# Kernel optimization log

Hardware: AMD Instinct MI355X
Metric: run time of the kernel (lower is better)

The kernel has to match this reference:

```python
import jax, jax.numpy as jnp
import numpy as np

B, C, H, W0, W1 = 2, 96, 64, 128, 128
NL, K, R = 2, 4, 6  # num_layers, cross-scan directions, dt_rank = ceil(C/16)
PNAMES = ['norm_w','norm_b','in_proj_w','conv_w','x_proj_w','dt_w','dt_b','A_logs','Ds',
          'out_norm_w','out_norm_b','out_proj_w','norm2_w','norm2_b','fc1_w','fc1_b','fc2_w','fc2_b']


def setup_inputs() -> dict:
    key = jax.random.key(0)
    ks = iter(jax.random.split(key, 40))
    def rn(shape, s=0.02):
        return jax.random.normal(next(ks), shape, jnp.float32) * s
    return dict(
        x0=jax.random.normal(next(ks), (B, C, H, W0), jnp.float32),
        x1=jax.random.normal(next(ks), (B, C, H, W1), jnp.float32),
        norm_w=jnp.ones((NL, C)), norm_b=jnp.zeros((NL, C)),
        in_proj_w=rn((NL, C, C)),                 # SS2D in_proj (Linear2d, bias=False)
        conv_w=rn((NL, C, 1, 3, 3), 0.1),         # depthwise 3x3, bias=False
        x_proj_w=rn((NL, K, R + 2, C)),           # dt_rank + 2*d_state rows (d_state=1)
        dt_w=rn((NL, K, C, R), 0.1),
        dt_b=rn((NL, K, C), 0.1),
        A_logs=jnp.zeros((NL, K, C)),             # v0 init with d_state=1 -> log(1)=0
        Ds=jnp.ones((NL, K, C)),
        out_norm_w=jnp.ones((NL, C)), out_norm_b=jnp.zeros((NL, C)),
        out_proj_w=rn((NL, C, C)),                # bias=False
        norm2_w=jnp.ones((NL, C)), norm2_b=jnp.zeros((NL, C)),
        fc1_w=rn((NL, 4 * C, C)), fc1_b=jnp.zeros((NL, 4 * C)),
        fc2_w=rn((NL, C, 4 * C)), fc2_b=jnp.zeros((NL, C)),
    )


def ln2d(x, w, b, eps=1e-5):
    # LayerNorm2d: normalize over channel dim of NCHW
    mu = x.mean(1, keepdims=True)
    var = ((x - mu) ** 2).mean(1, keepdims=True)
    return (x - mu) * jax.lax.rsqrt(var + eps) * w[None, :, None, None] + b[None, :, None, None]


def conv1x1(x, w):  # Linear2d: w (out,in)
    return jnp.einsum('bchw,dc->bdhw', x, w)


def dwconv3(x, w):  # depthwise 3x3, SAME padding
    return jax.lax.conv_general_dilated(x, w, (1, 1), 'SAME',
        dimension_numbers=('NCHW', 'OIHW', 'NCHW'), feature_group_count=x.shape[1])


def linear_scan(a, b):
    # h_t = a_t * h_{t-1} + b_t along last axis, via associative scan
    def comb(l, r):
        al, bl = l
        ar, br = r
        return (ar * al, ar * bl + br)
    return jax.lax.associative_scan(comb, (a, b), axis=-1)[1]


def ss2d(x, p):
    # SS2Dv2 forward_type='v05_noz', channel_first, d_state=1
    Bs_, Cd, Hh, Ww = x.shape
    Ll = Hh * Ww
    x = conv1x1(x, p['in_proj_w'])
    x = jax.nn.silu(dwconv3(x, p['conv_w']))
    # CrossScan: row-major, col-major, and their flips -> (B,K,C,L)
    xs0 = x.reshape(Bs_, Cd, Ll)
    xs1 = x.transpose(0, 1, 3, 2).reshape(Bs_, Cd, Ll)
    xs = jnp.stack([xs0, xs1, xs0[..., ::-1], xs1[..., ::-1]], 1)
    xdbl = jnp.einsum('bkcl,kdc->bkdl', xs, p['x_proj_w'])
    dts, Bmat, Cmat = xdbl[:, :, :R], xdbl[:, :, R:R + 1], xdbl[:, :, R + 1:R + 2]
    delta = jax.nn.softplus(jnp.einsum('bkrl,kcr->bkcl', dts, p['dt_w']) + p['dt_b'][None, :, :, None])
    A = -jnp.exp(p['A_logs'])                       # (K,C), scalar state
    a = jnp.exp(delta * A[None, :, :, None])        # (B,K,C,L)
    bterm = delta * Bmat * xs                       # Bmat broadcasts over C (d_state=1)
    h = linear_scan(a, bterm)
    ys = Cmat * h + p['Ds'][None, :, :, None] * xs  # (B,K,C,L)
    # CrossMerge: un-flip dirs 2,3; map col-major back to row-major; sum
    y_row = ys[:, 0] + ys[:, 2, :, ::-1]
    y_col = ys[:, 1] + ys[:, 3, :, ::-1]
    y_col = y_col.reshape(Bs_, Cd, Ww, Hh).transpose(0, 1, 3, 2).reshape(Bs_, Cd, Ll)
    y = (y_row + y_col).reshape(Bs_, Cd, Hh, Ww)
    y = ln2d(y, p['out_norm_w'], p['out_norm_b'])
    return conv1x1(y, p['out_proj_w'])


def block(x, p):
    # drop_path is identity in eval mode; all dropout rates are 0
    x = x + ss2d(ln2d(x, p['norm_w'], p['norm_b']), p)
    h = conv1x1(ln2d(x, p['norm2_w'], p['norm2_b']), p['fc1_w']) + p['fc1_b'][None, :, None, None]
    h = jax.nn.gelu(h, approximate=False)
    return x + conv1x1(h, p['fc2_w']) + p['fc2_b'][None, :, None, None]


def run_stack(x, params):
    for i in range(NL):
        p = {k: v[i] for k, v in params.items()}
        x = block(x, p)
    return x


def _forward(x0, x1, params):
    x = jnp.concatenate([x0, x1], -1)
    xb = x[..., ::-1]
    x = run_stack(x, params)
    xb = run_stack(xb, params)
    xbf = xb[..., ::-1]
    w0 = x0.shape[-1]
    y0 = 0.5 * (x[..., :w0] + xbf[..., :w0])
    y1 = 0.5 * (x[..., w0:] + xbf[..., w0:])
    return (y0, y1)


def reference(x0, x1, norm_w, norm_b, in_proj_w, conv_w, x_proj_w, dt_w, dt_b, A_logs, Ds,
              out_norm_w, out_norm_b, out_proj_w, norm2_w, norm2_b, fc1_w, fc1_b, fc2_w, fc2_b):
    params = dict(zip(PNAMES, [norm_w, norm_b, in_proj_w, conv_w, x_proj_w, dt_w, dt_b, A_logs, Ds,
                               out_norm_w, out_norm_b, out_proj_w, norm2_w, norm2_b, fc1_w, fc1_b, fc2_w, fc2_b]))
    return _forward(x0, x1, params)
```

## Files before the change

kernel.cpp:

```cpp
#include <hip/hip_runtime.h>
#include <cstdint>
#include <cstddef>

#define BT 4
#define CC 96
#define HH 64
#define WW 256
#define LL (HH*WW)
#define KD 4
#define RR 6
#define NLAY 2
#define C4 (4*CC)
#define SLOTF 47424
#define STPW 2048

typedef unsigned short u16;
typedef __attribute__((ext_vector_type(8))) short bf16x8;
typedef __attribute__((ext_vector_type(4))) float f32x4;

__device__ __forceinline__ u16 f2bf(float f){
  unsigned u = __float_as_uint(f);
  unsigned r = (u + 0x7FFFu + ((u >> 16) & 1u)) >> 16;
  return (u16)r;
}
__device__ __forceinline__ float bf2f(u16 h){
  return __uint_as_float(((unsigned)h) << 16);
}
__device__ __forceinline__ unsigned pk_bf16(float lo, float hi){
  unsigned r;
  asm volatile("v_cvt_pk_bf16_f32 %0, %1, %2" : "=v"(r) : "v"(lo), "v"(hi));
  return r;
}
__device__ __forceinline__ float fexp2(float x){
  float r; asm("v_exp_f32 %0, %1" : "=v"(r) : "v"(x)); return r;
}
__device__ __forceinline__ float flog2(float x){
  float r; asm("v_log_f32 %0, %1" : "=v"(r) : "v"(x)); return r;
}
__device__ __forceinline__ float gelu_f(float v){
  float t = v*v;
  float u = v*fmaf(0.0356774081f, t, 0.7978845608f);
  float e2 = __expf(2.f*u);
  float r = __builtin_amdgcn_rcpf(e2 + 1.f);
  return fmaf(-v, r, v);
}

__global__ void k_build(const float* __restrict__ x0, const float* __restrict__ x1,
                        float* __restrict__ X){
  size_t i = (size_t)blockIdx.x*256 + threadIdx.x;
  size_t tot = (size_t)2*CC*HH*WW;
  if (i >= tot) return;
  int w = i % WW; size_t r = i / WW;
  int h = r % HH; size_t bc = r / HH;
  float val;
  if (w < 128) val = x0[(bc*HH + h)*128 + w];
  else         val = x1[(bc*HH + h)*128 + (w-128)];
  X[i] = val;
  size_t ib = ((bc + (size_t)2*CC)*HH + h)*WW + (WW-1-w);
  X[ib] = val;
}

template<bool ST, typename T>
__global__ __launch_bounds__(256) void k_pack(const T* __restrict__ src,
      u16* __restrict__ dst, float* __restrict__ st){
  __shared__ float tl[CC][33];
  int tid = threadIdx.x;
  int l0 = blockIdx.x*32, b = blockIdx.y;
  for (int e = tid; e < CC*32; e += 256){
    int c = e >> 5, dl = e & 31;
    T raw = src[((size_t)b*CC + c)*LL + l0 + dl];
    float vv;
    if constexpr (sizeof(T) == 2) vv = bf2f((u16)raw); else vv = (float)raw;
    tl[c][dl] = vv;
  }
  __syncthreads();
  if (ST && tid < 32){
    float s = 0.f, ss = 0.f;
    for (int c = 0; c < CC; ++c){ float vv = tl[c][tid]; s += vv; ss += vv*vv; }
    float mu = s*(1.f/CC);
    float var = ss*(1.f/CC) - mu*mu;
    st[(size_t)b*LL + l0 + tid] = mu;
    st[(size_t)BT*LL + (size_t)b*LL + l0 + tid] = rsqrtf(var + 1e-5f);
  }
  int dl = tid >> 3, cg = tid & 7;
  u16* dp = dst + ((size_t)b*LL + l0 + dl)*104 + cg*12;
  #pragma unroll
  for (int q = 0; q < 3; ++q){
    ushort4 pk;
    pk.x = f2bf(tl[cg*12 + q*4 + 0][dl]);
    pk.y = f2bf(tl[cg*12 + q*4 + 1][dl]);
    pk.z = f2bf(tl[cg*12 + q*4 + 2][dl]);
    pk.w = f2bf(tl[cg*12 + q*4 + 3][dl]);
    *(ushort4*)(dp + q*4) = pk;
  }
}

template<int M, int K, bool FC1ORD, bool LNF, bool BIAS>
__global__ void k_prepw(const float* __restrict__ W, const float* __restrict__ lnw,
      const float* __restrict__ lnb, const float* __restrict__ bias,
      u16* __restrict__ Wb, float* __restrict__ s1, float* __restrict__ cadd){
  int lay = blockIdx.y;
  W += (size_t)lay*M*K;
  Wb += (size_t)lay*SLOTF*2;
  s1 += (size_t)lay*SLOTF;
  cadd += (size_t)lay*SLOTF;
  int m = blockIdx.x*64 + threadIdx.x;
  if (m >= M) return;
  int rowfrag = m >> 4, lr = m & 15;
  float s1v = 0.f, sbv = 0.f;
  for (int c = 0; c < K; ++c){
    float wv = W[(size_t)m*K + c];
    float wf = LNF ? wv*lnw[lay*K + c] : wv;
    u16 h = f2bf(wf);
    int colfrag = c >> 5, lg = (c >> 3) & 3, j = c & 7;
    int f;
    if (FC1ORD) f = (rowfrag/6)*18 + colfrag*6 + (rowfrag % 6);
    else        f = colfrag*(M/16) + rowfrag;
    Wb[(size_t)(f*64 + lg*16 + lr)*8 + j] = h;
    s1v += bf2f(h);
    if (LNF) sbv = fmaf(wv, lnb[lay*K + c], sbv);
  }
  if (BIAS) sbv += bias[lay*M + m];
  s1[m] = s1v;
  cadd[m] = sbv;
}

template<bool LNF, bool RES, bool WF32, bool WBF, bool STATS>
__global__ __launch_bounds__(256) void k_gmm2(
    const u16* __restrict__ Wb, const u16* __restrict__ inT,
    float* __restrict__ outF, u16* __restrict__ outT,
    const float* __restrict__ s1v, const float* __restrict__ cadd,
    const float* __restrict__ res,
    const float* __restrict__ stI, float* __restrict__ stO){
  __shared__ u16 bt[128*104];
  int tid = threadIdx.x, lane = tid & 63, wid = tid >> 6;
  int l0 = blockIdx.x*128;
  int lr = lane & 15, lg = lane >> 4;
  const int4* bsrc = (const int4*)(inT + (size_t)l0*104);
  for (int i = tid; i < 1664; i += 256) ((int4*)bt)[i] = bsrc[i];
  __syncthreads();
  f32x4 acc[6][2];
  #pragma unroll
  for (int mf = 0; mf < 6; ++mf){ acc[mf][0] = (f32x4){0,0,0,0}; acc[mf][1] = (f32x4){0,0,0,0}; }
  #pragma unroll
  for (int ks = 0; ks < 3; ++ks){
    bf16x8 af[6];
    #pragma unroll
    for (int mf = 0; mf < 6; ++mf)
      af[mf] = *(const bf16x8*)(Wb + (size_t)((ks*6 + mf)*64 + lane)*8);
    bf16x8 bfr[2];
    #pragma unroll
    for (int ls = 0; ls < 2; ++ls)
      bfr[ls] = *(const bf16x8*)&bt[(wid*32 + ls*16 + lr)*104 + ks*32 + lg*8];
    #pragma unroll
    for (int mf = 0; mf < 6; ++mf)
      #pragma unroll
      for (int ls = 0; ls < 2; ++ls)
        acc[mf][ls] = __builtin_amdgcn_mfma_f32_16x16x32_bf16(af[mf], bfr[ls], acc[mf][ls], 0, 0, 0);
  }
  #pragma unroll
  for (int ls = 0; ls < 2; ++ls){
    int l = l0 + wid*32 + ls*16 + lr;
    int b = l >> 14, lb = l & (LL-1);
    float mu = 0.f, rs = 0.f;
    if (LNF){ mu = stI[l]; rs = stI[(size_t)BT*LL + l]; }
    float ssum = 0.f, ssq = 0.f;
    #pragma unroll
    for (int mf = 0; mf < 6; ++mf){
      float o[4];
      #pragma unroll
      for (int r = 0; r < 4; ++r){
        int mm = mf*16 + lg*4 + r;
        float vv = acc[mf][ls][r];
        if (LNF) vv = fmaf(rs, vv, fmaf(-mu*rs, s1v[mm], cadd[mm]));
        else     vv += cadd[mm];
        if (RES) vv += res[((size_t)b*96 + mm)*LL + lb];
        if (WF32) outF[((size_t)b*96 + mm)*LL + lb] = vv;
        if (STATS){ ssum += vv; ssq += vv*vv; }
        o[r] = vv;
      }
      if (WBF){
        ushort4 pk;
        pk.x = f2bf(o[0]); pk.y = f2bf(o[1]); pk.z = f2bf(o[2]); pk.w = f2bf(o[3]);
        *(ushort4*)(outT + (size_t)l*104 + mf*16 + lg*4) = pk;
      }
    }
    if (STATS){
      ssum += __shfl_xor(ssum, 16); ssq += __shfl_xor(ssq, 16);
      ssum += __shfl_xor(ssum, 32); ssq += __shfl_xor(ssq, 32);
      if (lane < 16){
        float mu2 = ssum*(1.f/CC);
        float var = ssq*(1.f/CC) - mu2*mu2;
        stO[l] = mu2;
        stO[(size_t)BT*LL + l] = rsqrtf(var + 1e-5f);
      }
    }
  }
}

__global__ __launch_bounds__(512, 4) void k_mlp(
    const u16* __restrict__ Wb1, const u16* __restrict__ Wb2,
    const u16* __restrict__ XT, float* __restrict__ X, u16* __restrict__ XTout,
    const float* __restrict__ s11, const float* __restrict__ c1,
    const float* __restrict__ c2,
    const float* __restrict__ stI, float* __restrict__ stO){
  __shared__ u16 bt[128*104];
  __shared__ u16 hs[128*104];
  int tid = threadIdx.x, lane = tid & 63, wid = tid >> 6;
  int l0 = blockIdx.x*128;
  int lr = lane & 15, lg = lane >> 4;
  const int4* bsrc = (const int4*)(XT + (size_t)l0*104);
  for (int i = tid; i < 1664; i += 512) ((int4*)bt)[i] = bsrc[i];

  int l = l0 + wid*16 + lr;
  float mu = stI[l];
  float rs = stI[(size_t)BT*LL + l];
  float nmr = -mu*rs;
  __syncthreads();

  int hrow = (wid*16 + lr)*104;
  f32x4 acc2[6];
  #pragma unroll
  for (int mf = 0; mf < 6; ++mf) acc2[mf] = (f32x4){0,0,0,0};

  for (int cc = 0; cc < 4; ++cc){
    f32x4 acc1[6];
    #pragma unroll
    for (int mf = 0; mf < 6; ++mf) acc1[mf] = (f32x4){0,0,0,0};
    #pragma unroll
    for (int ks = 0; ks < 3; ++ks){
      bf16x8 af[6];
      #pragma unroll
      for (int mf = 0; mf < 6; ++mf)
        af[mf] = *(const bf16x8*)(Wb1 + (size_t)((cc*18 + ks*6 + mf)*64 + lane)*8);
      bf16x8 bfr = *(const bf16x8*)&bt[hrow + ks*32 + lg*8];
      #pragma unroll
      for (int mf = 0; mf < 6; ++mf)
        acc1[mf] = __builtin_amdgcn_mfma_f32_16x16x32_bf16(af[mf], bfr, acc1[mf], 0, 0, 0);
    }
    #pragma unroll
    for (int mf = 0; mf < 6; ++mf){
      float4 sv = *(const float4*)&s11[cc*96 + mf*16 + lg*4];
      float4 cv = *(const float4*)&c1 [cc*96 + mf*16 + lg*4];
      float g0 = gelu_f(fmaf(rs, acc1[mf][0], fmaf(nmr, sv.x, cv.x)));
      float g1 = gelu_f(fmaf(rs, acc1[mf][1], fmaf(nmr, sv.y, cv.y)));
      float g2 = gelu_f(fmaf(rs, acc1[mf][2], fmaf(nmr, sv.z, cv.z)));
      float g3 = gelu_f(fmaf(rs, acc1[mf][3], fmaf(nmr, sv.w, cv.w)));
      uint2 pw;
      pw.x = pk_bf16(g0, g1);
      pw.y = pk_bf16(g2, g3);
      *(uint2*)&hs[hrow + mf*16 + lg*4] = pw;
    }
    #pragma unroll
    for (int ks = 0; ks < 3; ++ks){
      bf16x8 a2[6];
      #pragma unroll
      for (int mf2 = 0; mf2 < 6; ++mf2)
        a2[mf2] = *(const bf16x8*)(Wb2 + (size_t)(((cc*3 + ks)*6 + mf2)*64 + lane)*8);
      bf16x8 bfr2 = *(const bf16x8*)&hs[hrow + ks*32 + lg*8];
      #pragma unroll
      for (int mf2 = 0; mf2 < 6; ++mf2)
        acc2[mf2] = __builtin_amdgcn_mfma_f32_16x16x32_bf16(a2[mf2], bfr2, acc2[mf2], 0, 0, 0);
    }
  }
  {
    int b = l >> 14, lb = l & (LL-1);
    float ssum = 0.f, ssq = 0.f;
    #pragma unroll
    for (int mf = 0; mf < 6; ++mf){
      float o[4];
      #pragma unroll
      for (int r = 0; r < 4; ++r){
        int mm = mf*16 + lg*4 + r;
        float vv = acc2[mf][r] + c2[mm];
        vv += X[((size_t)b*96 + mm)*LL + lb];
        X[((size_t)b*96 + mm)*LL + lb] = vv;
        ssum += vv; ssq += vv*vv;
        o[r] = vv;
      }
      ushort4 pk;
      pk.x = f2bf(o[0]); pk.y = f2bf(o[1]); pk.z = f2bf(o[2]); pk.w = f2bf(o[3]);
      *(ushort4*)(XTout + (size_t)l*104 + mf*16 + lg*4) = pk;
    }
    ssum += __shfl_xor(ssum, 16); ssq += __shfl_xor(ssq, 16);
    ssum += __shfl_xor(ssum, 32); ssq += __shfl_xor(ssq, 32);
    if (lane < 16){
      float mu2 = ssum*(1.f/CC);
      float var = ssq*(1.f/CC) - mu2*mu2;
      stO[l] = mu2;
      stO[(size_t)BT*LL + l] = rsqrtf(var + 1e-5f);
    }
  }
}

__global__ __launch_bounds__(256) void k_dwconv_silu_t(const float* __restrict__ u,
      float* __restrict__ v, float* __restrict__ vT, const float* __restrict__ cw){
  __shared__ float tl[32][33];
  int bc = blockIdx.z;
  int c = bc % CC;
  int w0 = blockIdx.x*32, h0 = blockIdx.y*32;
  const float* up = u + (size_t)bc*LL;
  const float* k9 = cw + c*9;
  int t = threadIdx.x;
  int wl = (t & 7)*4, hl = t >> 3;
  int h = h0 + hl, w = w0 + wl;
  float acc[4] = {0.f,0.f,0.f,0.f};
  #pragma unroll
  for (int dh = -1; dh <= 1; ++dh){
    int h2 = h + dh;
    if (h2 < 0 || h2 >= HH) continue;
    const float* row = up + (size_t)h2*WW + w;
    float4 m = *(const float4*)row;
    float lft = (w > 0) ? row[-1] : 0.f;
    float rgt = (w + 4 < WW) ? row[4] : 0.f;
    float k0 = k9[(dh+1)*3], k1 = k9[(dh+1)*3+1], k2 = k9[(dh+1)*3+2];
    acc[0] += lft*k0 + m.x*k1 + m.y*k2;
    acc[1] += m.x*k0 + m.y*k1 + m.z*k2;
    acc[2] += m.y*k0 + m.z*k1 + m.w*k2;
    acc[3] += m.z*k0 + m.w*k1 + rgt*k2;
  }
  float4 ov;
  float* po = (float*)&ov;
  #pragma unroll
  for (int j = 0; j < 4; ++j){
    float a = acc[j];
    float e = __expf(-a);
    float s = a * __builtin_amdgcn_rcpf(1.f + e);
    po[j] = s;
    tl[wl + j][hl] = s;
  }
  *(float4*)&v[(size_t)bc*LL + (size_t)h*WW + w] = ov;
  __syncthreads();
  int ww = t >> 3, hh4 = (t & 7)*4;
  float4 o2 = make_float4(tl[ww][hh4], tl[ww][hh4+1], tl[ww][hh4+2], tl[ww][hh4+3]);
  *(float4*)&vT[(size_t)bc*LL + (size_t)(w0 + ww)*HH + h0 + hh4] = o2;
}

__global__ void k_xproj(const float* __restrict__ v, const float* __restrict__ vT,
                        float* __restrict__ G, const float* __restrict__ xpw){
  int which = blockIdx.y;
  const float* src = which ? vT : v;
  int kA = which ? 1 : 0, kB = which ? 3 : 2;
  size_t i = (size_t)blockIdx.x*256 + threadIdx.x;
  if (i >= (size_t)BT*LL) return;
  int b = (int)(i / LL), l = (int)(i % LL);
  const float* sp = src + (size_t)b*CC*LL + l;
  const float* wA = xpw + (size_t)kA*8*CC;
  const float* wB = xpw + (size_t)kB*8*CC;
  float aA[8], aB[8];
  #pragma unroll
  for (int d = 0; d < 8; ++d){ aA[d] = 0.f; aB[d] = 0.f; }
  for (int c = 0; c < CC; ++c){
    float xv = sp[(size_t)c*LL];
    #pragma unroll
    for (int d = 0; d < 8; ++d){
      aA[d] = fmaf(wA[d*CC + c], xv, aA[d]);
      aB[d] = fmaf(wB[d*CC + c], xv, aB[d]);
    }
  }
  float* gA = G + (((size_t)b*KD + kA)*8)*LL + l;
  float* gB = G + (((size_t)b*KD + kB)*8)*LL + l;
  #pragma unroll
  for (int d = 0; d < 8; ++d){ gA[(size_t)d*LL] = aA[d]; gB[(size_t)d*LL] = aB[d]; }
}

__device__ __forceinline__ void ld4(const float* p, float* o){
  float4 t = *(const float4*)p; o[0]=t.x; o[1]=t.y; o[2]=t.z; o[3]=t.w;
}
__device__ __forceinline__ void rev4(float* a){
  float t0 = a[0]; a[0] = a[3]; a[3] = t0;
  float t1 = a[1]; a[1] = a[2]; a[2] = t1;
}

__global__ __launch_bounds__(256) void k_scan3(const float* __restrict__ G,
                       const float* __restrict__ v, const float* __restrict__ vT,
                       u16* __restrict__ Y,
                       const float* __restrict__ dtw_, const float* __restrict__ dtb_,
                       const float* __restrict__ Alog_, const float* __restrict__ Ds_){
  const size_t SZ = (size_t)BT*CC*LL;
  const float LOG2E = 1.4426950408889634f, LN2 = 0.6931471805599453f;
  int wid = threadIdx.x >> 6, lane = threadIdx.x & 63;
  int tile = blockIdx.x*4 + wid;
  int sy = blockIdx.y;
  bool rev = (blockIdx.z != 0);
  int c = sy % CC; int t2 = sy / CC; int kk = t2 & 1; int b = t2 >> 1;
  int k = (rev ? 2 : 0) + kk;
  const float* src = (kk ? vT : v) + ((size_t)b*CC + c)*LL;
  const float* g = G + (((size_t)b*KD + k)*8)*LL;
  float dtw[RR];
  #pragma unroll
  for (int r = 0; r < RR; ++r) dtw[r] = dtw_[((size_t)k*CC + c)*RR + r];
  float dtb = dtb_[k*CC + c];
  float A  = -__expf(Alog_[k*CC + c]);
  float Dv = Ds_[k*CC + c];
  u16* yout = Y + (size_t)k*SZ + ((size_t)b*CC + c)*LL;

  int lstore0 = tile*STPW;
  float carry = 0.f;
  for (int p = 0; p < 1 + STPW/256; ++p){
    int base = lstore0 - 256 + p*256;
    if (base < 0) continue;
    bool st = (base >= lstore0);
    int l = base + (lane<<2);
    int ga = rev ? (LL-4-l) : l;
    float r0[4], r1[4], r2[4], r3[4], r4[4], r5[4], g6b[4], g7b[4], xb[4];
    ld4(g + 0*(size_t)LL + ga, r0);
    ld4(g + 1*(size_t)LL + ga, r1);
    ld4(g + 2*(size_t)LL + ga, r2);
    ld4(g + 3*(size_t)LL + ga, r3);
    ld4(g + 4*(size_t)LL + ga, r4);
    ld4(g + 5*(size_t)LL + ga, r5);
    ld4(g + 6*(size_t)LL + ga, g6b);
    if (st) ld4(g + 7*(size_t)LL + ga, g7b);
    else { g7b[0]=0.f; g7b[1]=0.f; g7b[2]=0.f; g7b[3]=0.f; }
    ld4(src + ga, xb);
    if (rev){
      rev4(r0); rev4(r1); rev4(r2); rev4(r3); rev4(r4); rev4(r5);
      rev4(g6b); rev4(g7b); rev4(xb);
    }
    float av[4], bt[4];
    #pragma unroll
    for (int i = 0; i < 4; ++i){
      float dsum = dtb;
      dsum = fmaf(r0[i], dtw[0], dsum);
      dsum = fmaf(r1[i], dtw[1], dsum);
      dsum = fmaf(r2[i], dtw[2], dsum);
      dsum = fmaf(r3[i], dtw[3], dsum);
      dsum = fmaf(r4[i], dtw[4], dsum);
      dsum = fmaf(r5[i], dtw[5], dsum);
      float dl2 = dsum*LOG2E;
      float y = flog2(1.f + fexp2(dl2));
      y = (dsum > 20.f) ? dl2 : y;
      float delta = y*LN2;
      av[i] = fexp2(A*y);
      bt[i] = delta * g6b[i] * xb[i];
    }
    float P = av[0], Q = bt[0];
    #pragma unroll
    for (int i = 1; i < 4; ++i){ Q = fmaf(av[i], Q, bt[i]); P *= av[i]; }
    #pragma unroll
    for (int off = 1; off < 64; off <<= 1){
      float Pp = __shfl_up(P, (unsigned)off);
      float Qp = __shfl_up(Q, (unsigned)off);
      if (lane >= off){ Q = fmaf(P, Qp, Q); P *= Pp; }
    }
    float Pe = __shfl_up(P, 1u), Qe = __shfl_up(Q, 1u);
    if (lane == 0){ Pe = 1.f; Qe = 0.f; }
    float h = fmaf(Pe, carry, Qe);
    if (st){
      float ys[4];
      #pragma unroll
      for (int i = 0; i < 4; ++i){
        h = fmaf(av[i], h, bt[i]);
        ys[i] = fmaf(g7b[i], h, Dv*xb[i]);
      }
      carry = __shfl(h, 63);
      if (rev) rev4(ys);
      uint2 pw;
      pw.x = pk_bf16(ys[0], ys[1]);
      pw.y = pk_bf16(ys[2], ys[3]);
      *(uint2*)&yout[ga] = pw;
    } else {
      #pragma unroll
      for (int i = 0; i < 4; ++i) h = fmaf(av[i], h, bt[i]);
      carry = __shfl(h, 63);
    }
  }
}

__global__ __launch_bounds__(256) void k_combine4(const u16* __restrict__ Y, u16* __restrict__ z){
  const size_t SZ = (size_t)BT*CC*LL;
  __shared__ float tl[64][65];
  int bc = blockIdx.z;
  int w0 = blockIdx.x*64;
  int t = threadIdx.x;
  const u16* y1p = Y + SZ   + (size_t)bc*LL;
  const u16* y3p = Y + 3*SZ + (size_t)bc*LL;
  {
    int wl = t >> 2;
    int h0 = (t & 3)*16;
    size_t base = (size_t)(w0 + wl)*HH + h0;
    #pragma unroll
    for (int j = 0; j < 4; ++j){
      ushort4 a = *(const ushort4*)&y1p[base + j*4];
      ushort4 bq = *(const ushort4*)&y3p[base + j*4];
      tl[wl][h0 + j*4 + 0] = bf2f(a.x) + bf2f(bq.x);
      tl[wl][h0 + j*4 + 1] = bf2f(a.y) + bf2f(bq.y);
      tl[wl][h0 + j*4 + 2] = bf2f(a.z) + bf2f(bq.z);
      tl[wl][h0 + j*4 + 3] = bf2f(a.w) + bf2f(bq.w);
    }
  }
  __syncthreads();
  const u16* y0p = Y +        (size_t)bc*LL;
  const u16* y2p = Y + 2*SZ + (size_t)bc*LL;
  u16* zp = z + (size_t)bc*LL;
  {
    int h = t >> 2;
    int wq = (t & 3)*16;
    #pragma unroll
    for (int j = 0; j < 4; ++j){
      int wl = wq + j*4;
      size_t idx = (size_t)h*WW + w0 + wl;
      ushort4 a = *(const ushort4*)&y0p[idx];
      ushort4 bq = *(const ushort4*)&y2p[idx];
      ushort4 o;
      o.x = f2bf(bf2f(a.x) + bf2f(bq.x) + tl[wl+0][h]);
      o.y = f2bf(bf2f(a.y) + bf2f(bq.y) + tl[wl+1][h]);
      o.z = f2bf(bf2f(a.z) + bf2f(bq.z) + tl[wl+2][h]);
      o.w = f2bf(bf2f(a.w) + bf2f(bq.w) + tl[wl+3][h]);
      *(ushort4*)&zp[idx] = o;
    }
  }
}

__global__ void k_output(const float* __restrict__ X, float* __restrict__ out){
  size_t i = (size_t)blockIdx.x*256 + threadIdx.x;
  size_t half = (size_t)2*CC*HH*128;
  if (i >= half) return;
  int w = i % 128; size_t r = i / 128;
  int h = r % HH; size_t bc = r / HH;
  size_t fwd = (bc*HH + h)*WW;
  size_t bwd = ((bc + (size_t)2*CC)*HH + h)*WW;
  out[i]        = 0.5f*(X[fwd + w]       + X[bwd + (WW-1-w)]);
  out[half + i] = 0.5f*(X[fwd + 128 + w] + X[bwd + (127 - w)]);
}

extern "C" void kernel_launch(void* const* d_in, const int* in_sizes, int n_in,
                              void* d_out, int out_size, void* d_ws, size_t ws_size,
                              hipStream_t stream){
  const float* x0        = (const float*)d_in[0];
  const float* x1        = (const float*)d_in[1];
  const float* norm_w    = (const float*)d_in[2];
  const float* norm_b    = (const float*)d_in[3];
  const float* in_proj_w = (const float*)d_in[4];
  const float* conv_w    = (const float*)d_in[5];
  const float* x_proj_w  = (const float*)d_in[6];
  const float* dt_w      = (const float*)d_in[7];
  const float* dt_b      = (const float*)d_in[8];
  const float* A_logs    = (const float*)d_in[9];
  const float* Ds        = (const float*)d_in[10];
  const float* out_norm_w= (const float*)d_in[11];
  const float* out_norm_b= (const float*)d_in[12];
  const float* out_proj_w= (const float*)d_in[13];
  const float* norm2_w   = (const float*)d_in[14];
  const float* norm2_b   = (const float*)d_in[15];
  const float* fc1_w     = (const float*)d_in[16];
  const float* fc1_b     = (const float*)d_in[17];
  const float* fc2_w     = (const float*)d_in[18];
  const float* fc2_b     = (const float*)d_in[19];

  const size_t SZ = (size_t)BT*CC*LL;
  float* X  = (float*)d_ws;
  float* t  = X + SZ;
  float* u  = t + SZ;
  float* G  = u + SZ;
  float* v  = G + (size_t)BT*KD*8*LL;
  float* vT = v + SZ;
  float* Yf = vT + SZ;
  u16*   Yb = (u16*)Yf;
  u16*   XT = (u16*)Yf;
  u16*   tB = (u16*)t;
  u16*   tT = (u16*)u;
  float* ext = Yf + 4*SZ;
  float* stats_X = ext;
  float* stats_t = stats_X + 2*(size_t)BT*LL;
  float* wsl     = stats_t + 2*(size_t)BT*LL;

  float* p0 = wsl;
  u16*  WbI0 = (u16*)p0;          float* s1I0 = p0 + 4608;  float* cI0 = p0 + 4704;
  u16*  WbO0 = (u16*)(p0+4800);   float* s1O0 = p0 + 9408;  float* cO0 = p0 + 9504;
  u16*  Wb10 = (u16*)(p0+9600);   float* s110 = p0 + 28032; float* c10 = p0 + 28416;
  u16*  Wb20 = (u16*)(p0+28800);  float* s120 = p0 + 47232; float* c20 = p0 + 47328;

  k_prepw<96,96,false,true,false><<<dim3(2,NLAY),64,0,stream>>>(in_proj_w, norm_w, norm_b, nullptr, WbI0, s1I0, cI0);
  k_prepw<96,96,false,true,false><<<dim3(2,NLAY),64,0,stream>>>(out_proj_w, out_norm_w, out_norm_b, nullptr, WbO0, s1O0, cO0);
  k_prepw<384,96,true,true,true><<<dim3(6,NLAY),64,0,stream>>>(fc1_w, norm2_w, norm2_b, fc1_b, Wb10, s110, c10);
  k_prepw<96,384,false,false,true><<<dim3(2,NLAY),64,0,stream>>>(fc2_w, nullptr, nullptr, fc2_b, Wb20, s120, c20);

  k_build<<<(2*CC*HH*WW + 255)/256, 256, 0, stream>>>(x0, x1, X);
  k_pack<true,float><<<dim3(LL/32, BT), 256, 0, stream>>>(X, XT, stats_X);

  for (int lay = 0; lay < NLAY; ++lay){
    size_t so = (size_t)lay*SLOTF;
    const u16* WbI = WbI0 + so*2; const float* s1I = s1I0 + so; const float* cI = cI0 + so;
    const u16* WbO = WbO0 + so*2; const float* s1O = s1O0 + so; const float* cO = cO0 + so;
    const u16* Wb1 = Wb10 + so*2; const float* s11 = s110 + so; const float* c1 = c10 + so;
    const u16* Wb2 = Wb20 + so*2; const float* c2 = c20 + so;
    const float* cw  = conv_w    + (size_t)lay*CC*9;
    const float* xpw = x_proj_w  + (size_t)lay*KD*8*CC;
    const float* dw  = dt_w      + (size_t)lay*KD*CC*RR;
    const float* db  = dt_b      + (size_t)lay*KD*CC;
    const float* Al  = A_logs    + (size_t)lay*KD*CC;
    const float* Dp  = Ds        + (size_t)lay*KD*CC;

    k_gmm2<true,false,true,false,false><<<dim3(BT*LL/128),256,0,stream>>>(
        WbI, XT, u, nullptr, s1I, cI, nullptr, stats_X, nullptr);
    k_dwconv_silu_t<<<dim3(8,2,BT*CC), 256, 0, stream>>>(u, v, vT, cw);
    k_xproj<<<dim3(BT*LL/256, 2), 256, 0, stream>>>(v, vT, G, xpw);
    k_scan3<<<dim3(2,768,2), 256, 0, stream>>>(G, v, vT, Yb, dw, db, Al, Dp);
    k_combine4<<<dim3(4,1,BT*CC), 256, 0, stream>>>(Yb, tB);
    k_pack<true,u16><<<dim3(LL/32, BT), 256, 0, stream>>>(tB, tT, stats_t);
    k_gmm2<true,true,true,true,true><<<dim3(BT*LL/128),256,0,stream>>>(
        WbO, tT, X, XT, s1O, cO, X, stats_t, stats_X);
    k_mlp<<<dim3(BT*LL/128),512,0,stream>>>(
        Wb1, Wb2, XT, X, XT, s11, c1, c2, stats_X, stats_X);
  }

  k_output<<<(unsigned)(((size_t)2*CC*HH*128 + 255)/256), 256, 0, stream>>>(X, (float*)d_out);
}
```

Baseline: 422.3 us.

## Store in_proj output and conv/SiLU activations as bf16 across SS2D stages

Switches the in_proj output u, the depthwise-conv/SiLU output v, and its transpose vT from fp32 to bf16 storage. The in_proj GEMM writes bf16 directly, and the dwconv, x_proj and scan kernels read bf16 and convert to float. This halves the memory traffic of these large intermediate tensors, at the cost of reduced precision in the scan inputs and x_proj. Whether pk_bf16 is defined in the hidden part of the file cannot be confirmed.

```diff
diff --git a/kernel.cpp b/kernel.cpp
--- a/kernel.cpp
+++ b/kernel.cpp
@@ -125,13 +125,14 @@
   cadd[m] = sbv;
 }
 
-template<bool LNF, bool RES, bool WF32, bool WBF, bool STATS>
+template<bool LNF, bool RES, bool WF32, bool WBF, bool STATS, bool WPB>
 __global__ __launch_bounds__(256) void k_gmm2(
     const u16* __restrict__ Wb, const u16* __restrict__ inT,
     float* __restrict__ outF, u16* __restrict__ outT,
     const float* __restrict__ s1v, const float* __restrict__ cadd,
     const float* __restrict__ res,
-    const float* __restrict__ stI, float* __restrict__ stO){
+    const float* __restrict__ stI, float* __restrict__ stO,
+    u16* __restrict__ outPB){
   __shared__ u16 bt[128*104];
   int tid = threadIdx.x, lane = tid & 63, wid = tid >> 6;
   int l0 = blockIdx.x*128;
@@ -176,6 +177,7 @@
         else     vv += cadd[mm];
         if (RES) vv += res[((size_t)b*96 + mm)*LL + lb];
         if (WF32) outF[((size_t)b*96 + mm)*LL + lb] = vv;
+        if (WPB)  outPB[((size_t)b*96 + mm)*LL + lb] = f2bf(vv);
         if (STATS){ ssum += vv; ssq += vv*vv; }
         o[r] = vv;
       }
@@ -293,13 +295,13 @@
   }
 }
 
-__global__ __launch_bounds__(256) void k_dwconv_silu_t(const float* __restrict__ u,
-      float* __restrict__ v, float* __restrict__ vT, const float* __restrict__ cw){
+__global__ __launch_bounds__(256) void k_dwconv_silu_t(const u16* __restrict__ u,
+      u16* __restrict__ v, u16* __restrict__ vT, const float* __restrict__ cw){
   __shared__ float tl[32][33];
   int bc = blockIdx.z;
   int c = bc % CC;
   int w0 = blockIdx.x*32, h0 = blockIdx.y*32;
-  const float* up = u + (size_t)bc*LL;
+  const u16* up = u + (size_t)bc*LL;
   const float* k9 = cw + c*9;
   int t = threadIdx.x;
   int wl = (t & 7)*4, hl = t >> 3;
@@ -309,49 +311,53 @@
   for (int dh = -1; dh <= 1; ++dh){
     int h2 = h + dh;
     if (h2 < 0 || h2 >= HH) continue;
-    const float* row = up + (size_t)h2*WW + w;
-    float4 m = *(const float4*)row;
-    float lft = (w > 0) ? row[-1] : 0.f;
-    float rgt = (w + 4 < WW) ? row[4] : 0.f;
+    const u16* row = up + (size_t)h2*WW + w;
+    ushort4 mq = *(const ushort4*)row;
+    float m0 = bf2f(mq.x), m1 = bf2f(mq.y), m2 = bf2f(mq.z), m3 = bf2f(mq.w);
+    float lft = (w > 0) ? bf2f(row[-1]) : 0.f;
+    float rgt = (w + 4 < WW) ? bf2f(row[4]) : 0.f;
     float k0 = k9[(dh+1)*3], k1 = k9[(dh+1)*3+1], k2 = k9[(dh+1)*3+2];
-    acc[0] += lft*k0 + m.x*k1 + m.y*k2;
-    acc[1] += m.x*k0 + m.y*k1 + m.z*k2;
-    acc[2] += m.y*k0 + m.z*k1 + m.w*k2;
-    acc[3] += m.z*k0 + m.w*k1 + rgt*k2;
-  }
-  float4 ov;
-  float* po = (float*)&ov;
+    acc[0] += lft*k0 + m0*k1 + m1*k2;
+    acc[1] += m0*k0 + m1*k1 + m2*k2;
+    acc[2] += m1*k0 + m2*k1 + m3*k2;
+    acc[3] += m2*k0 + m3*k1 + rgt*k2;
+  }
+  float s[4];
   #pragma unroll
   for (int j = 0; j < 4; ++j){
     float a = acc[j];
     float e = __expf(-a);
-    float s = a * __builtin_amdgcn_rcpf(1.f + e);
-    po[j] = s;
-    tl[wl + j][hl] = s;
-  }
-  *(float4*)&v[(size_t)bc*LL + (size_t)h*WW + w] = ov;
+    s[j] = a * __builtin_amdgcn_rcpf(1.f + e);
+    tl[wl + j][hl] = s[j];
+  }
+  uint2 pw;
+  pw.x = pk_bf16(s[0], s[1]);
+  pw.y = pk_bf16(s[2], s[3]);
+  *(uint2*)&v[(size_t)bc*LL + (size_t)h*WW + w] = pw;
   __syncthreads();
   int ww = t >> 3, hh4 = (t & 7)*4;
-  float4 o2 = make_float4(tl[ww][hh4], tl[ww][hh4+1], tl[ww][hh4+2], tl[ww][hh4+3]);
-  *(float4*)&vT[(size_t)bc*LL + (size_t)(w0 + ww)*HH + h0 + hh4] = o2;
-}
-
-__global__ void k_xproj(const float* __restrict__ v, const float* __restrict__ vT,
+  uint2 po;
+  po.x = pk_bf16(tl[ww][hh4],   tl[ww][hh4+1]);
+  po.y = pk_bf16(tl[ww][hh4+2], tl[ww][hh4+3]);
+  *(uint2*)&vT[(size_t)bc*LL + (size_t)(w0 + ww)*HH + h0 + hh4] = po;
+}
+
+__global__ void k_xproj(const u16* __restrict__ v, const u16* __restrict__ vT,
                         float* __restrict__ G, const float* __restrict__ xpw){
   int which = blockIdx.y;
-  const float* src = which ? vT : v;
+  const u16* src = which ? vT : v;
   int kA = which ? 1 : 0, kB = which ? 3 : 2;
   size_t i = (size_t)blockIdx.x*256 + threadIdx.x;
   if (i >= (size_t)BT*LL) return;
   int b = (int)(i / LL), l = (int)(i % LL);
-  const float* sp = src + (size_t)b*CC*LL + l;
+  const u16* sp = src + (size_t)b*CC*LL + l;
   const float* wA = xpw + (size_t)kA*8*CC;
   const float* wB = xpw + (size_t)kB*8*CC;
   float aA[8], aB[8];
   #pragma unroll
   for (int d = 0; d < 8; ++d){ aA[d] = 0.f; aB[d] = 0.f; }
   for (int c = 0; c < CC; ++c){
-    float xv = sp[(size_t)c*LL];
+    float xv = bf2f(sp[(size_t)c*LL]);
     #pragma unroll
     for (int d = 0; d < 8; ++d){
       aA[d] = fmaf(wA[d*CC + c], xv, aA[d]);
@@ -367,13 +373,17 @@
 __device__ __forceinline__ void ld4(const float* p, float* o){
   float4 t = *(const float4*)p; o[0]=t.x; o[1]=t.y; o[2]=t.z; o[3]=t.w;
 }
+__device__ __forceinline__ void ldb4(const u16* p, float* o){
+  ushort4 t = *(const ushort4*)p;
+  o[0]=bf2f(t.x); o[1]=bf2f(t.y); o[2]=bf2f(t.z); o[3]=bf2f(t.w);
+}
 __device__ __forceinline__ void rev4(float* a){
   float t0 = a[0]; a[0] = a[3]; a[3] = t0;
   float t1 = a[1]; a[1] = a[2]; a[2] = t1;
 }
 
 __global__ __launch_bounds__(256) void k_scan3(const float* __restrict__ G,
-                       const float* __restrict__ v, const float* __restrict__ vT,
+                       const u16* __restrict__ v, const u16* __restrict__ vT,
                        u16* __restrict__ Y,
                        const float* __restrict__ dtw_, const float* __restrict__ dtb_,
                        const float* __restrict__ Alog_, const float* __restrict__ Ds_){
@@ -385,7 +395,7 @@
   bool rev = (blockIdx.z != 0);
   int c = sy % CC; int t2 = sy / CC; int kk = t2 & 1; int b = t2 >> 1;
   int k = (rev ? 2 : 0) + kk;
-  const float* src = (kk ? vT : v) + ((size_t)b*CC + c)*LL;
+  const u16* src = (kk ? vT : v) + ((size_t)b*CC + c)*LL;
   const float* g = G + (((size_t)b*KD + k)*8)*LL;
   float dtw[RR];
   #pragma unroll
@@ -413,7 +423,7 @@
     ld4(g + 6*(size_t)LL + ga, g6b);
     if (st) ld4(g + 7*(size_t)LL + ga, g7b);
     else { g7b[0]=0.f; g7b[1]=0.f; g7b[2]=0.f; g7b[3]=0.f; }
-    ld4(src + ga, xb);
+    ldb4(src + ga, xb);
     if (rev){
       rev4(r0); rev4(r1); rev4(r2); rev4(r3); rev4(r4); rev4(r5);
       rev4(g6b); rev4(g7b); rev4(xb);
@@ -559,6 +569,9 @@
   float* Yf = vT + SZ;
   u16*   Yb = (u16*)Yf;
   u16*   XT = (u16*)Yf;
+  u16*   uB = (u16*)u;
+  u16*   vB = (u16*)v;
+  u16*   vTB= (u16*)vT;
   u16*   tB = (u16*)t;
   u16*   tT = (u16*)u;
   float* ext = Yf + 4*SZ;
@@ -593,15 +606,15 @@
     const float* Al  = A_logs    + (size_t)lay*KD*CC;
     const float* Dp  = Ds        + (size_t)lay*KD*CC;
 
-    k_gmm2<true,false,true,false,false><<<dim3(BT*LL/128),256,0,stream>>>(
-        WbI, XT, u, nullptr, s1I, cI, nullptr, stats_X, nullptr);
-    k_dwconv_silu_t<<<dim3(8,2,BT*CC), 256, 0, stream>>>(u, v, vT, cw);
-    k_xproj<<<dim3(BT*LL/256, 2), 256, 0, stream>>>(v, vT, G, xpw);
-    k_scan3<<<dim3(2,768,2), 256, 0, stream>>>(G, v, vT, Yb, dw, db, Al, Dp);
+    k_gmm2<true,false,false,false,false,true><<<dim3(BT*LL/128),256,0,stream>>>(
+        WbI, XT, nullptr, nullptr, s1I, cI, nullptr, stats_X, nullptr, uB);
+    k_dwconv_silu_t<<<dim3(8,2,BT*CC), 256, 0, stream>>>(uB, vB, vTB, cw);
+    k_xproj<<<dim3(BT*LL/256, 2), 256, 0, stream>>>(vB, vTB, G, xpw);
+    k_scan3<<<dim3(2,768,2), 256, 0, stream>>>(G, vB, vTB, Yb, dw, db, Al, Dp);
     k_combine4<<<dim3(4,1,BT*CC), 256, 0, stream>>>(Yb, tB);
     k_pack<true,u16><<<dim3(LL/32, BT), 256, 0, stream>>>(tB, tT, stats_t);
-    k_gmm2<true,true,true,true,true><<<dim3(BT*LL/128),256,0,stream>>>(
-        WbO, tT, X, XT, s1O, cO, X, stats_t, stats_X);
+    k_gmm2<true,true,true,true,true,false><<<dim3(BT*LL/128),256,0,stream>>>(
+        WbO, tT, X, XT, s1O, cO, X, stats_t, stats_X, nullptr);
     k_mlp<<<dim3(BT*LL/128),512,0,stream>>>(
         Wb1, Wb2, XT, X, XT, s11, c1, c2, stats_X, stats_X);
   }
```

Result: no change. 421.0 us (-0.3%).
